# Kernel tuning notes

Hardware: AMD Instinct MI355X
Metric: run time of the kernel (lower is better)

Reference implementation:

```python
import jax, jax.numpy as jnp
import numpy as np
import math

M, DIN, DTGT = 65536, 256, 256   # feature count and feature dims
S, SD_IN, SD_TGT = 64, 256, 256  # num_slots, in_slot_dim, tgt_slot_dim
ITERS = 3
H_IN = 128                        # mlp_in hidden (hardcoded 128 in source)
H_TGT = SD_TGT if SD_TGT > 128 else 128  # mlp_tgt hidden

ARGS = ["inputs", "target", "in_slots", "tgt_slots",
        "ln_in_g", "ln_in_b", "ln_tgt_g", "ln_tgt_b",
        "Wk", "bk", "Wv", "bv", "Wvt", "bvt",
        "ln_slots_g", "ln_slots_b", "Wq", "bq",
        "gru_in_Wih", "gru_in_Whh", "gru_in_bih", "gru_in_bhh",
        "gru_tgt_Wih", "gru_tgt_Whh", "gru_tgt_bih", "gru_tgt_bhh",
        "ln_mi_g", "ln_mi_b", "mi_W1", "mi_b1", "mi_W2", "mi_b2",
        "ln_mt_g", "ln_mt_b", "mt_W1", "mt_b1", "mt_W2", "mt_b2"]


def _ln(x, g, b):
    m = jnp.mean(x, axis=-1, keepdims=True)
    v = jnp.var(x, axis=-1, keepdims=True)
    return (x - m) * jax.lax.rsqrt(v + 1e-5) * g + b


def _gru(x, h, Wih, Whh, bih, bhh):
    # torch.nn.GRUCell semantics; Wih: (D, 3H), Whh: (H, 3H)
    H = h.shape[-1]
    gi = x @ Wih + bih
    gh = h @ Whh + bhh
    r = jax.nn.sigmoid(gi[:, :H] + gh[:, :H])
    z = jax.nn.sigmoid(gi[:, H:2 * H] + gh[:, H:2 * H])
    n = jnp.tanh(gi[:, 2 * H:] + r * gh[:, 2 * H:])
    return (1.0 - z) * n + z * h


def _forward(inputs, target, in_slots, tgt_slots,
             ln_in_g, ln_in_b, ln_tgt_g, ln_tgt_b,
             Wk, bk, Wv, bv, Wvt, bvt,
             ln_slots_g, ln_slots_b, Wq, bq,
             gru_in_Wih, gru_in_Whh, gru_in_bih, gru_in_bhh,
             gru_tgt_Wih, gru_tgt_Whh, gru_tgt_bih, gru_tgt_bhh,
             ln_mi_g, ln_mi_b, mi_W1, mi_b1, mi_W2, mi_b2,
             ln_mt_g, ln_mt_b, mt_W1, mt_b1, mt_W2, mt_b2):
    inputs_norm = _ln(inputs, ln_in_g, ln_in_b)          # [M, DIN]
    in_k = inputs_norm @ Wk + bk                          # [M, SD_IN]
    in_v = inputs_norm @ Wv + bv                          # [M, SD_IN]
    tgt_v = _ln(target, ln_tgt_g, ln_tgt_b) @ Wvt + bvt   # [M, SD_TGT]
    scale = 1.0 / math.sqrt(in_k.shape[1])
    attn = None
    for _ in range(ITERS):
        q = _ln(in_slots, ln_slots_g, ln_slots_b) @ Wq + bq   # [S, SD_IN]
        logits = (q @ in_k.T) * scale                          # [S, M]
        attn = jax.nn.softmax(logits, axis=0)                  # softmax over SLOTS (dim=0)
        in_up = attn @ in_v                                    # [S, SD_IN]
        tgt_up = attn @ tgt_v                                  # [S, SD_TGT]
        in_slots = _gru(in_up, in_slots, gru_in_Wih, gru_in_Whh, gru_in_bih, gru_in_bhh)
        tgt_slots = _gru(tgt_up, tgt_slots, gru_tgt_Wih, gru_tgt_Whh, gru_tgt_bih, gru_tgt_bhh)
        in_slots = in_slots + (jax.nn.relu(_ln(in_slots, ln_mi_g, ln_mi_b) @ mi_W1 + mi_b1) @ mi_W2 + mi_b2)
        tgt_slots = tgt_slots + (jax.nn.relu(_ln(tgt_slots, ln_mt_g, ln_mt_b) @ mt_W1 + mt_b1) @ mt_W2 + mt_b2)
    return (in_slots, tgt_slots, attn)


def setup_inputs() -> dict:
    key = jax.random.key(0)
    ks = iter(jax.random.split(key, 64))
    rn = lambda shape, s=1.0: jax.random.normal(next(ks), shape, dtype=jnp.float32) * s
    w = 0.02
    d = {
        "inputs": rn((M, DIN)),
        "target": rn((M, DTGT)),
        "in_slots": rn((S, SD_IN)),
        "tgt_slots": rn((S, SD_TGT)),
        "ln_in_g": jnp.ones((DIN,)), "ln_in_b": jnp.zeros((DIN,)),
        "ln_tgt_g": jnp.ones((DTGT,)), "ln_tgt_b": jnp.zeros((DTGT,)),
        "Wk": rn((DIN, SD_IN), w), "bk": jnp.zeros((SD_IN,)),
        "Wv": rn((DIN, SD_IN), w), "bv": jnp.zeros((SD_IN,)),
        "Wvt": rn((DTGT, SD_TGT), w), "bvt": jnp.zeros((SD_TGT,)),
        "ln_slots_g": jnp.ones((SD_IN,)), "ln_slots_b": jnp.zeros((SD_IN,)),
        "Wq": rn((SD_IN, SD_IN), w), "bq": jnp.zeros((SD_IN,)),
        "gru_in_Wih": rn((SD_IN, 3 * SD_IN), w), "gru_in_Whh": rn((SD_IN, 3 * SD_IN), w),
        "gru_in_bih": jnp.zeros((3 * SD_IN,)), "gru_in_bhh": jnp.zeros((3 * SD_IN,)),
        "gru_tgt_Wih": rn((SD_TGT, 3 * SD_TGT), w), "gru_tgt_Whh": rn((SD_TGT, 3 * SD_TGT), w),
        "gru_tgt_bih": jnp.zeros((3 * SD_TGT,)), "gru_tgt_bhh": jnp.zeros((3 * SD_TGT,)),
        "ln_mi_g": jnp.ones((SD_IN,)), "ln_mi_b": jnp.zeros((SD_IN,)),
        "mi_W1": rn((SD_IN, H_IN), w), "mi_b1": jnp.zeros((H_IN,)),
        "mi_W2": rn((H_IN, SD_IN), w), "mi_b2": jnp.zeros((SD_IN,)),
        "ln_mt_g": jnp.ones((SD_TGT,)), "ln_mt_b": jnp.zeros((SD_TGT,)),
        "mt_W1": rn((SD_TGT, H_TGT), w), "mt_b1": jnp.zeros((H_TGT,)),
        "mt_W2": rn((H_TGT, SD_TGT), w), "mt_b2": jnp.zeros((SD_TGT,)),
    }
    return {k: d[k] for k in ARGS}


def reference(inputs, target, in_slots, tgt_slots,
              ln_in_g, ln_in_b, ln_tgt_g, ln_tgt_b,
              Wk, bk, Wv, bv, Wvt, bvt,
              ln_slots_g, ln_slots_b, Wq, bq,
              gru_in_Wih, gru_in_Whh, gru_in_bih, gru_in_bhh,
              gru_tgt_Wih, gru_tgt_Whh, gru_tgt_bih, gru_tgt_bhh,
              ln_mi_g, ln_mi_b, mi_W1, mi_b1, mi_W2, mi_b2,
              ln_mt_g, ln_mt_b, mt_W1, mt_b1, mt_W2, mt_b2):
    return _forward(inputs, target, in_slots, tgt_slots,
                    ln_in_g, ln_in_b, ln_tgt_g, ln_tgt_b,
                    Wk, bk, Wv, bv, Wvt, bvt,
                    ln_slots_g, ln_slots_b, Wq, bq,
                    gru_in_Wih, gru_in_Whh, gru_in_bih, gru_in_bhh,
                    gru_tgt_Wih, gru_tgt_Whh, gru_tgt_bih, gru_tgt_bhh,
                    ln_mi_g, ln_mi_b, mi_W1, mi_b1, mi_W2, mi_b2,
                    ln_mt_g, ln_mt_b, mt_W1, mt_b1, mt_W2, mt_b2)
```

## Files before the change

kernel.cpp:

```cpp
#include <hip/hip_runtime.h>
#include <hip/hip_bf16.h>
#include <math.h>

typedef __bf16 bf16_t;
typedef __bf16 bf16x8 __attribute__((ext_vector_type(8)));
typedef __bf16 bf16x4 __attribute__((ext_vector_type(4)));
typedef float f32x4 __attribute__((ext_vector_type(4)));

#define DEVI __device__ __forceinline__

DEVI f32x4 mfma16(bf16x8 a, bf16x8 b, f32x4 c) {
  return __builtin_amdgcn_mfma_f32_16x16x32_bf16(a, b, c, 0, 0, 0);
}
DEVI bf16x8 ld8(const bf16_t* p) { return *reinterpret_cast<const bf16x8*>(p); }


struct WtArgs { const float* s0; const float* s1; const float* s2; const float* s3;
                const float* s4; const float* s5; const float* s6; const float* s7;
                const float* s8; const float* s9; const float* s10; const float* s11; };

__global__ __launch_bounds__(256) void k_wtrans(WtArgs A, bf16_t* __restrict__ wt) {
  constexpr int offs[12] = {0,65536,131072,196608,262144,458752,655360,851968,
                            1048576,1081344,1114112,1179648};
  constexpr int Ks[12]   = {256,256,256,256,256,256,256,256,256,128,256,256};
  constexpr int Ns[12]   = {256,256,256,256,768,768,768,768,128,256,256,256};
  const int m = blockIdx.y;
  const int K = Ks[m], N = Ns[m];
  const int tn = N >> 6;
  const int tile = blockIdx.x;
  if (tile >= (K >> 6) * tn) return;
  const int tk = tile / tn, tc = tile - tk * tn;
  const float* sp;
  switch (m) {
    case 0: sp = A.s0; break; case 1: sp = A.s1; break; case 2: sp = A.s2; break;
    case 3: sp = A.s3; break; case 4: sp = A.s4; break; case 5: sp = A.s5; break;
    case 6: sp = A.s6; break; case 7: sp = A.s7; break; case 8: sp = A.s8; break;
    case 9: sp = A.s9; break; case 10: sp = A.s10; break; default: sp = A.s11; break;
  }
  __shared__ float ts[64][65];
  const int t = threadIdx.x;
  const int k0 = tk * 64, n0 = tc * 64;
  {
    const int c = t & 63, rq = t >> 6;
    #pragma unroll
    for (int i = 0; i < 16; ++i) {
      const int r = rq * 16 + i;
      ts[r][c] = sp[(size_t)(k0 + r) * N + n0 + c];
    }
  }
  __syncthreads();
  bf16_t* dst = wt + offs[m];
  const int n_l = t & 63, kq = t >> 6;
  #pragma unroll
  for (int h = 0; h < 2; ++h) {
    const int k_l = kq * 16 + h * 8;
    bf16x8 pk;
    #pragma unroll
    for (int e = 0; e < 8; ++e) pk[e] = (bf16_t)ts[k_l + e][n_l];
    const int n_g = n0 + n_l, k_g = k0 + k_l;
    const int nt = n_g >> 4, kc = k_g >> 5;
    const int lane = (((k_g >> 3) & 3) << 4) + (n_g & 15);
    *reinterpret_cast<bf16x8*>(dst + (((size_t)(nt * (K >> 5) + kc)) << 9) + lane * 8) = pk;
  }
}

__global__ __launch_bounds__(256) void k_init(const float* __restrict__ in_slots,
                                              const float* __restrict__ tgt_slots,
                                              float* __restrict__ h_f32,
                                              bf16_t* __restrict__ h_bf) {
  int idx = blockIdx.x * 256 + threadIdx.x;
  int side = idx >> 14, j = idx & 16383;
  int s = j >> 8, d = j & 255;
  float x = (side ? tgt_slots : in_slots)[j];
  h_f32[idx] = x;
  h_bf[side*16384 + (((s>>4)*8 + (d>>5))<<9) + ((d>>3)&3)*128 + (s&15)*8 + (d&7)] = (bf16_t)x;
}

__global__ __launch_bounds__(256) void k_phaseA(
    const float* __restrict__ inputs, const float* __restrict__ target,
    const float* __restrict__ ln_in_g, const float* __restrict__ ln_in_b,
    const float* __restrict__ ln_tgt_g, const float* __restrict__ ln_tgt_b,
    const bf16_t* __restrict__ wkF, const bf16_t* __restrict__ wvF, const bf16_t* __restrict__ wvtF,
    const float* __restrict__ bk, const float* __restrict__ bv, const float* __restrict__ bvt,
    bf16_t* __restrict__ in_kF, bf16_t* __restrict__ in_vF, bf16_t* __restrict__ tgt_vF) {
  const int side = blockIdx.y;
  const int m0 = blockIdx.x * 64;
  const int t = threadIdx.x, l = t & 63, w = t >> 6;
  __shared__ __align__(16) bf16_t anorm[64][264];
  const float* src = side ? target : inputs;
  const float* gp = side ? ln_tgt_g : ln_in_g;
  const float* bp = side ? ln_tgt_b : ln_in_b;
  const float4 g4 = *reinterpret_cast<const float4*>(gp + l * 4);
  const float4 b4 = *reinterpret_cast<const float4*>(bp + l * 4);
  float4 v[16];
  #pragma unroll
  for (int i = 0; i < 16; ++i)
    v[i] = *reinterpret_cast<const float4*>(src + (size_t)(m0 + w*16 + i) * 256 + l * 4);
  #pragma unroll
  for (int i = 0; i < 16; ++i) {
    float s1 = v[i].x + v[i].y + v[i].z + v[i].w;
    float s2 = v[i].x*v[i].x + v[i].y*v[i].y + v[i].z*v[i].z + v[i].w*v[i].w;
    #pragma unroll
    for (int msk = 1; msk < 64; msk <<= 1) { s1 += __shfl_xor(s1, msk); s2 += __shfl_xor(s2, msk); }
    const float mean = s1 * (1.f/256.f);
    const float rstd = rsqrtf(s2 * (1.f/256.f) - mean*mean + 1e-5f);
    bf16x4 pk;
    pk[0] = (bf16_t)((v[i].x - mean) * rstd * g4.x + b4.x);
    pk[1] = (bf16_t)((v[i].y - mean) * rstd * g4.y + b4.y);
    pk[2] = (bf16_t)((v[i].z - mean) * rstd * g4.z + b4.z);
    pk[3] = (bf16_t)((v[i].w - mean) * rstd * g4.w + b4.w);
    *reinterpret_cast<bf16x4*>(&anorm[w*16 + i][l*4]) = pk;
  }
  __syncthreads();
  const int l16 = l & 15, l4 = l >> 4;
  const int e = l16 & 7, lh = l16 >> 3;

  if (side == 0) {
    f32x4 acc[4][4] = {};
    for (int ks = 0; ks < 8; ++ks) {
      const int k = ks*32 + l4*8;
      bf16x8 a[4], b[4];
      #pragma unroll
      for (int mi = 0; mi < 4; ++mi) a[mi] = ld8(&anorm[mi*16 + l16][k]);
      #pragma unroll
      for (int ni = 0; ni < 4; ++ni) b[ni] = ld8(wkF + (((size_t)((w*4 + ni)*8 + ks)) << 9) + l*8);
      #pragma unroll
      for (int mi = 0; mi < 4; ++mi)
        #pragma unroll
        for (int ni = 0; ni < 4; ++ni) acc[mi][ni] = mfma16(a[mi], b[ni], acc[mi][ni]);
    }
    #pragma unroll
    for (int mi = 0; mi < 4; ++mi)
      #pragma unroll
      for (int ni = 0; ni < 4; ++ni) {
        const int d = w*64 + ni*16 + l16;
        const float bias = bk[d];
        const int kc = w*2 + (ni >> 1);
        const int l4p = (ni & 1)*2 + lh;
        bf16_t* outp = in_kF + ((((size_t)(blockIdx.x*4 + mi))*8 + kc) << 9) + l4p*128 + e;
        #pragma unroll
        for (int rr = 0; rr < 4; ++rr)
          outp[(l4*4 + rr)*8] = (bf16_t)(acc[mi][ni][rr] + bias);
      }
  }
  {
    const bf16_t* WF = side ? wvtF : wvF;
    const float* bias = side ? bvt : bv;
    bf16_t* out = side ? tgt_vF : in_vF;
    f32x4 acc[4][4] = {};
    for (int ks = 0; ks < 8; ++ks) {
      const int k = ks*32 + l4*8;
      bf16x8 a[4], b[4];
      #pragma unroll
      for (int mi = 0; mi < 4; ++mi) a[mi] = ld8(WF + (((size_t)((w*4 + mi)*8 + ks)) << 9) + l*8);
      #pragma unroll
      for (int ni = 0; ni < 4; ++ni) b[ni] = ld8(&anorm[ni*16 + l16][k]);
      #pragma unroll
      for (int mi = 0; mi < 4; ++mi)
        #pragma unroll
        for (int ni = 0; ni < 4; ++ni) acc[mi][ni] = mfma16(a[mi], b[ni], acc[mi][ni]);
    }
    #pragma unroll
    for (int mi = 0; mi < 4; ++mi)
      #pragma unroll
      for (int ni = 0; ni < 4; ++ni) {
        const int dt = w*4 + mi;
        const int mc = blockIdx.x*2 + (ni >> 1);
        const int l4p = (ni & 1)*2 + lh;
        bf16_t* outp = out + ((((size_t)dt)*2048 + mc) << 9) + l4p*128 + e;
        #pragma unroll
        for (int rr = 0; rr < 4; ++rr) {
          const int d = w*64 + mi*16 + l4*4 + rr;
          outp[(l4*4 + rr)*8] = (bf16_t)(acc[mi][ni][rr] + bias[d]);
        }
      }
  }
}

__global__ __launch_bounds__(256) void k_q(
    const float* __restrict__ h_in,
    const float* __restrict__ ln_g, const float* __restrict__ ln_b,
    const bf16_t* __restrict__ wqF, const float* __restrict__ bq,
    bf16_t* __restrict__ q_bf) {
  __shared__ __align__(16) bf16_t anorm[64][264];
  const int t = threadIdx.x, l = t & 63, w = t >> 6;
  const float4 g4 = *reinterpret_cast<const float4*>(ln_g + l * 4);
  const float4 b4 = *reinterpret_cast<const float4*>(ln_b + l * 4);
  float4 v[16];
  #pragma unroll
  for (int i = 0; i < 16; ++i)
    v[i] = *reinterpret_cast<const float4*>(h_in + (size_t)(w*16 + i) * 256 + l * 4);
  #pragma unroll
  for (int i = 0; i < 16; ++i) {
    float s1 = v[i].x + v[i].y + v[i].z + v[i].w;
    float s2 = v[i].x*v[i].x + v[i].y*v[i].y + v[i].z*v[i].z + v[i].w*v[i].w;
    #pragma unroll
    for (int msk = 1; msk < 64; msk <<= 1) { s1 += __shfl_xor(s1, msk); s2 += __shfl_xor(s2, msk); }
    const float mean = s1 * (1.f/256.f);
    const float rstd = rsqrtf(s2 * (1.f/256.f) - mean*mean + 1e-5f);
    bf16x4 pk;
    pk[0] = (bf16_t)((v[i].x - mean) * rstd * g4.x + b4.x);
    pk[1] = (bf16_t)((v[i].y - mean) * rstd * g4.y + b4.y);
    pk[2] = (bf16_t)((v[i].z - mean) * rstd * g4.z + b4.z);
    pk[3] = (bf16_t)((v[i].w - mean) * rstd * g4.w + b4.w);
    *reinterpret_cast<bf16x4*>(&anorm[w*16 + i][l*4]) = pk;
  }
  __syncthreads();
  const int l16 = l & 15, l4 = l >> 4;
  f32x4 acc[4][4] = {};
  for (int ks = 0; ks < 8; ++ks) {
    const int k = ks*32 + l4*8;
    bf16x8 a[4], b[4];
    #pragma unroll
    for (int mi = 0; mi < 4; ++mi) a[mi] = ld8(&anorm[mi*16 + l16][k]);
    #pragma unroll
    for (int ni = 0; ni < 4; ++ni) b[ni] = ld8(wqF + (((size_t)((w*4 + ni)*8 + ks)) << 9) + l*8);
    #pragma unroll
    for (int mi = 0; mi < 4; ++mi)
      #pragma unroll
      for (int ni = 0; ni < 4; ++ni) acc[mi][ni] = mfma16(a[mi], b[ni], acc[mi][ni]);
  }
  #pragma unroll
  for (int mi = 0; mi < 4; ++mi)
    #pragma unroll
    for (int ni = 0; ni < 4; ++ni) {
      const int d = w*64 + ni*16 + l16;
      const float bias = bq[d];
      bf16_t* outp = q_bf + (((size_t)(mi*8 + w*2 + (ni>>1))) << 9) + ((ni&1)*2 + (l16>>3))*128 + (l16&7);
      #pragma unroll
      for (int rr = 0; rr < 4; ++rr)
        outp[(l4*4 + rr)*8] = (bf16_t)((acc[mi][ni][rr] + bias) * 0.0625f);
    }
}

__global__ __launch_bounds__(256) void k_logits(
    const bf16_t* __restrict__ q_bf, const bf16_t* __restrict__ in_kF,
    bf16_t* __restrict__ attnF, float* __restrict__ attn_f32, int write_f32) {
  const int t = threadIdx.x, l = t & 63, w = t >> 6, l16 = l & 15, l4 = l >> 4;
  const int m0 = blockIdx.x * 256 + w * 64;
  f32x4 acc[4][4] = {};
  for (int ks = 0; ks < 8; ++ks) {
    bf16x8 a[4], b[4];
    #pragma unroll
    for (int mi = 0; mi < 4; ++mi) a[mi] = ld8(q_bf + (((size_t)(mi*8 + ks)) << 9) + l*8);
    #pragma unroll
    for (int ni = 0; ni < 4; ++ni)
      b[ni] = ld8(in_kF + (((size_t)((blockIdx.x*16 + w*4 + ni)*8 + ks)) << 9) + l*8);
    #pragma unroll
    for (int mi = 0; mi < 4; ++mi)
      #pragma unroll
      for (int ni = 0; ni < 4; ++ni) acc[mi][ni] = mfma16(a[mi], b[ni], acc[mi][ni]);
  }
  #pragma unroll
  for (int ni = 0; ni < 4; ++ni) {
    float mx = -3.0e38f;
    #pragma unroll
    for (int mi = 0; mi < 4; ++mi)
      #pragma unroll
      for (int rr = 0; rr < 4; ++rr) mx = fmaxf(mx, acc[mi][ni][rr]);
    mx = fmaxf(mx, __shfl_xor(mx, 16));
    mx = fmaxf(mx, __shfl_xor(mx, 32));
    float sm = 0.f;
    #pragma unroll
    for (int mi = 0; mi < 4; ++mi)
      #pragma unroll
      for (int rr = 0; rr < 4; ++rr) {
        float ev = __expf(acc[mi][ni][rr] - mx);
        acc[mi][ni][rr] = ev; sm += ev;
      }
    sm += __shfl_xor(sm, 16);
    sm += __shfl_xor(sm, 32);
    const float inv = 1.0f / sm;
    #pragma unroll
    for (int mi = 0; mi < 4; ++mi)
      #pragma unroll
      for (int rr = 0; rr < 4; ++rr) acc[mi][ni][rr] *= inv;
  }
  #pragma unroll
  for (int mi = 0; mi < 4; ++mi)
    #pragma unroll
    for (int ni = 0; ni < 4; ++ni) {
      const int mc = blockIdx.x*8 + w*2 + (ni >> 1);
      bf16_t* outp = attnF + ((((size_t)mi)*2048 + mc) << 9) + ((ni&1)*2 + (l16>>3))*128 + (l16&7);
      #pragma unroll
      for (int rr = 0; rr < 4; ++rr) {
        outp[(l4*4 + rr)*8] = (bf16_t)acc[mi][ni][rr];
        if (write_f32) {
          const int s = mi*16 + l4*4 + rr;
          attn_f32[(size_t)s*65536 + (m0 + ni*16 + l16)] = acc[mi][ni][rr];
        }
      }
    }
}

__global__ __launch_bounds__(256) void k_pv(
    const bf16_t* __restrict__ attnF,
    const bf16_t* __restrict__ in_vF, const bf16_t* __restrict__ tgt_vF,
    bf16_t* __restrict__ p_in, bf16_t* __restrict__ p_tgt) {
  const int c = blockIdx.x, side = blockIdx.y;
  const bf16_t* V = side ? tgt_vF : in_vF;
  bf16_t* P = side ? p_tgt : p_in;
  const int t = threadIdx.x, l = t & 63, w = t >> 6, l16 = l & 15, l4 = l >> 4;
  f32x4 acc[4][4] = {};
  for (int ks = 0; ks < 16; ++ks) {
    const size_t mc = c*16 + ks;
    bf16x8 a[4], b[4];
    #pragma unroll
    for (int mi = 0; mi < 4; ++mi) a[mi] = ld8(attnF + ((((size_t)mi)*2048 + mc) << 9) + l*8);
    #pragma unroll
    for (int ni = 0; ni < 4; ++ni) b[ni] = ld8(V + ((((size_t)(w*4 + ni))*2048 + mc) << 9) + l*8);
    #pragma unroll
    for (int mi = 0; mi < 4; ++mi)
      #pragma unroll
      for (int ni = 0; ni < 4; ++ni) acc[mi][ni] = mfma16(a[mi], b[ni], acc[mi][ni]);
  }
  #pragma unroll
  for (int mi = 0; mi < 4; ++mi)
    #pragma unroll
    for (int ni = 0; ni < 4; ++ni) {
      const int d = w*64 + ni*16 + l16;
      #pragma unroll
      for (int rr = 0; rr < 4; ++rr) {
        const int s = mi*16 + l4*4 + rr;
        P[(size_t)c*16384 + s*256 + d] = (bf16_t)acc[mi][ni][rr];
      }
    }
}

__global__ __launch_bounds__(256) void k_pvred(
    const bf16_t* __restrict__ p_in, const bf16_t* __restrict__ p_tgt,
    bf16_t* __restrict__ upF) {
  const int b = blockIdx.x;
  const int side = b >> 6, s = b & 63;
  const int d = threadIdx.x;
  const bf16_t* P = (side ? p_tgt : p_in) + s*256 + d;
  float sum = 0.f;
  #pragma unroll 8
  for (int cc = 0; cc < 128; ++cc) sum += (float)P[(size_t)cc * 16384];
  upF[side*16384 + (((s>>4)*8 + (d>>5))<<9) + ((d>>3)&3)*128 + (s&15)*8 + (d&7)] = (bf16_t)sum;
}

__global__ __launch_bounds__(256) void k_gates(
    const bf16_t* __restrict__ upF, const bf16_t* __restrict__ h_bf,
    const bf16_t* __restrict__ wihF_in, const bf16_t* __restrict__ whhF_in,
    const bf16_t* __restrict__ wihF_tgt, const bf16_t* __restrict__ whhF_tgt,
    const float* __restrict__ bih_in, const float* __restrict__ bhh_in,
    const float* __restrict__ bih_tgt, const float* __restrict__ bhh_tgt,
    float* __restrict__ gi, float* __restrict__ gh) {
  const int nchunk = blockIdx.x, which = blockIdx.y, side = blockIdx.z;
  const bf16_t* Aop = (which ? h_bf : upF) + side*16384;
  const bf16_t* WF = side ? (which ? whhF_tgt : wihF_tgt) : (which ? whhF_in : wihF_in);
  const float* bias = side ? (which ? bhh_tgt : bih_tgt) : (which ? bhh_in : bih_in);
  float* out = (which ? gh : gi) + side*49152;
  const int t = threadIdx.x, l = t & 63, w = t >> 6, l16 = l & 15, l4 = l >> 4;
  const int n0 = nchunk*256 + w*64;
  f32x4 acc[4][4] = {};
  for (int ks = 0; ks < 8; ++ks) {
    bf16x8 a[4], b[4];
    #pragma unroll
    for (int mi = 0; mi < 4; ++mi) a[mi] = ld8(Aop + (((size_t)(mi*8 + ks)) << 9) + l*8);
    #pragma unroll
    for (int ni = 0; ni < 4; ++ni)
      b[ni] = ld8(WF + (((size_t)((nchunk*16 + w*4 + ni)*8 + ks)) << 9) + l*8);
    #pragma unroll
    for (int mi = 0; mi < 4; ++mi)
      #pragma unroll
      for (int ni = 0; ni < 4; ++ni) acc[mi][ni] = mfma16(a[mi], b[ni], acc[mi][ni]);
  }
  #pragma unroll
  for (int mi = 0; mi < 4; ++mi)
    #pragma unroll
    for (int ni = 0; ni < 4; ++ni) {
      const int n = n0 + ni*16 + l16;
      const float bb = bias[n];
      #pragma unroll
      for (int rr = 0; rr < 4; ++rr) {
        const int s = mi*16 + l4*4 + rr;
        out[(size_t)s*768 + n] = acc[mi][ni][rr] + bb;
      }
    }
}

__global__ __launch_bounds__(256) void k_gru_ln(
    const float* __restrict__ gi, const float* __restrict__ gh,
    const float* __restrict__ h_f32,
    const float* __restrict__ ln_mi_g, const float* __restrict__ ln_mi_b,
    const float* __restrict__ ln_mt_g, const float* __restrict__ ln_mt_b,
    float* __restrict__ hp_f32, bf16_t* __restrict__ hpnF) {
  const int s = blockIdx.x, side = blockIdx.y;
  const int d = threadIdx.x;
  const float* GI = gi + side*49152 + s*768;
  const float* GH = gh + side*49152 + s*768;
  const float hv = h_f32[side*16384 + s*256 + d];
  const float rg = 1.f / (1.f + __expf(-(GI[d] + GH[d])));
  const float zg = 1.f / (1.f + __expf(-(GI[256 + d] + GH[256 + d])));
  const float ng = tanhf(GI[512 + d] + rg * GH[512 + d]);
  const float hp = (1.f - zg) * ng + zg * hv;
  float a = hp, b2 = hp * hp;
  #pragma unroll
  for (int msk = 1; msk < 64; msk <<= 1) { a += __shfl_xor(a, msk); b2 += __shfl_xor(b2, msk); }
  __shared__ float reda[4], redb[4];
  const int w = d >> 6, lid = d & 63;
  if (lid == 0) { reda[w] = a; redb[w] = b2; }
  __syncthreads();
  const float S1 = reda[0] + reda[1] + reda[2] + reda[3];
  const float S2 = redb[0] + redb[1] + redb[2] + redb[3];
  const float mean = S1 * (1.f/256.f);
  const float rstd = rsqrtf(S2 * (1.f/256.f) - mean*mean + 1e-5f);
  const float* g = side ? ln_mt_g : ln_mi_g;
  const float* bb = side ? ln_mt_b : ln_mi_b;
  const float nv = (hp - mean) * rstd * g[d] + bb[d];
  hp_f32[side*16384 + s*256 + d] = hp;
  hpnF[side*16384 + (((s>>4)*8 + (d>>5))<<9) + ((d>>3)&3)*128 + (s&15)*8 + (d&7)] = (bf16_t)nv;
}

__global__ __launch_bounds__(256) void k_mlpq(
    const bf16_t* __restrict__ hpnF,
    const bf16_t* __restrict__ w1F_in, const bf16_t* __restrict__ w1F_tgt,
    const float* __restrict__ b1_in, const float* __restrict__ b1_tgt,
    const bf16_t* __restrict__ w2F_in, const bf16_t* __restrict__ w2F_tgt,
    const float* __restrict__ b2_in, const float* __restrict__ b2_tgt,
    const float* __restrict__ hp_f32,
    float* __restrict__ h_f32, bf16_t* __restrict__ h_bf, float* __restrict__ slots_out,
    const float* __restrict__ ln_sg, const float* __restrict__ ln_sb,
    const bf16_t* __restrict__ wqF, const float* __restrict__ bq,
    bf16_t* __restrict__ q_bf, int make_q) {
  const int side = blockIdx.x;
  __shared__ __align__(16) bf16_t hid[64][264];
  const int t = threadIdx.x, l = t & 63, w = t >> 6, l16 = l & 15, l4 = l >> 4;
  const int NH = side ? 256 : 128;
  {
    const bf16_t* Aop = hpnF + side*16384;
    const bf16_t* WF = side ? w1F_tgt : w1F_in;
    const float* b1 = side ? b1_tgt : b1_in;
    const int ntiles = NH >> 6;
    for (int nt = 0; nt < ntiles; ++nt) {
      const int n0 = w*(NH>>2) + nt*16;
      f32x4 acc[4] = {};
      for (int ks = 0; ks < 8; ++ks) {
        bf16x8 b = ld8(WF + (((size_t)((n0>>4)*8 + ks)) << 9) + l*8);
        #pragma unroll
        for (int mt = 0; mt < 4; ++mt)
          acc[mt] = mfma16(ld8(Aop + (((size_t)(mt*8 + ks)) << 9) + l*8), b, acc[mt]);
      }
      const float bb = b1[n0 + l16];
      #pragma unroll
      for (int mt = 0; mt < 4; ++mt)
        #pragma unroll
        for (int rr = 0; rr < 4; ++rr) {
          const int s = mt*16 + l4*4 + rr;
          hid[s][n0 + l16] = (bf16_t)fmaxf(acc[mt][rr] + bb, 0.f);
        }
    }
  }
  __syncthreads();
  {
    const bf16_t* WF = side ? w2F_tgt : w2F_in;
    const float* b2 = side ? b2_tgt : b2_in;
    const int ksteps = NH >> 5;
    #pragma unroll
    for (int nt = 0; nt < 4; ++nt) {
      const int n0 = w*64 + nt*16;
      f32x4 acc[4] = {};
      for (int ks = 0; ks < ksteps; ++ks) {
        const int k = ks*32 + l4*8;
        bf16x8 b = ld8(WF + (((size_t)((n0>>4)*ksteps + ks)) << 9) + l*8);
        #pragma unroll
        for (int mt = 0; mt < 4; ++mt)
          acc[mt] = mfma16(ld8(&hid[mt*16 + l16][k]), b, acc[mt]);
      }
      const int n = n0 + l16;
      const float bb = b2[n];
      #pragma unroll
      for (int mt = 0; mt < 4; ++mt)
        #pragma unroll
        for (int rr = 0; rr < 4; ++rr) {
          const int s = mt*16 + l4*4 + rr;
          const int idx = side*16384 + s*256 + n;
          const float val = acc[mt][rr] + bb + hp_f32[idx];
          h_f32[idx] = val;
          slots_out[idx] = val;
          h_bf[side*16384 + (((s>>4)*8 + (n>>5))<<9) + ((n>>3)&3)*128 + (s&15)*8 + (n&7)] = (bf16_t)val;
        }
    }
  }
  if (!make_q || side != 0) return;
  __syncthreads();
  {
    for (int i = 0; i < 16; ++i) {
      const int s = w*16 + i;
      float4 x = *reinterpret_cast<const float4*>(h_f32 + s*256 + 4*l);
      float a = x.x + x.y + x.z + x.w;
      float b2s = x.x*x.x + x.y*x.y + x.z*x.z + x.w*x.w;
      #pragma unroll
      for (int msk = 1; msk < 64; msk <<= 1) { a += __shfl_xor(a, msk); b2s += __shfl_xor(b2s, msk); }
      const float mean = a * (1.f/256.f);
      const float rstd = rsqrtf(b2s * (1.f/256.f) - mean*mean + 1e-5f);
      float4 g4 = *reinterpret_cast<const float4*>(ln_sg + 4*l);
      float4 bb4 = *reinterpret_cast<const float4*>(ln_sb + 4*l);
      bf16x4 pk;
      pk[0] = (bf16_t)((x.x - mean) * rstd * g4.x + bb4.x);
      pk[1] = (bf16_t)((x.y - mean) * rstd * g4.y + bb4.y);
      pk[2] = (bf16_t)((x.z - mean) * rstd * g4.z + bb4.z);
      pk[3] = (bf16_t)((x.w - mean) * rstd * g4.w + bb4.w);
      *reinterpret_cast<bf16x4*>(&hid[s][4*l]) = pk;
    }
  }
  __syncthreads();
  {
    #pragma unroll
    for (int nt = 0; nt < 4; ++nt) {
      const int n0 = w*64 + nt*16;
      f32x4 acc[4] = {};
      for (int ks = 0; ks < 8; ++ks) {
        const int k = ks*32 + l4*8;
        bf16x8 b = ld8(wqF + (((size_t)((n0>>4)*8 + ks)) << 9) + l*8);
        #pragma unroll
        for (int mt = 0; mt < 4; ++mt)
          acc[mt] = mfma16(ld8(&hid[mt*16 + l16][k]), b, acc[mt]);
      }
      const int d = n0 + l16;
      const float bb = bq[d];
      bf16_t* outp = q_bf + (((size_t)(0)) ) ;
      #pragma unroll
      for (int mt = 0; mt < 4; ++mt) {
        bf16_t* op = q_bf + (((size_t)(mt*8 + (d>>5))) << 9) + ((d>>3)&3)*128 + (d&7);
        #pragma unroll
        for (int rr = 0; rr < 4; ++rr)
          op[(l4*4 + rr)*8] = (bf16_t)((acc[mt][rr] + bb) * 0.0625f);
      }
      (void)outp;
    }
  }
}

extern "C" void kernel_launch(void* const* d_in, const int* in_sizes, int n_in,
                              void* d_out, int out_size, void* d_ws, size_t ws_size,
                              hipStream_t stream) {
  (void)in_sizes; (void)n_in; (void)out_size; (void)ws_size;
  const float* inputs     = (const float*)d_in[0];
  const float* target     = (const float*)d_in[1];
  const float* in_slots   = (const float*)d_in[2];
  const float* tgt_slots  = (const float*)d_in[3];
  const float* ln_in_g    = (const float*)d_in[4];
  const float* ln_in_b    = (const float*)d_in[5];
  const float* ln_tgt_g   = (const float*)d_in[6];
  const float* ln_tgt_b   = (const float*)d_in[7];
  const float* Wk  = (const float*)d_in[8];
  const float* bk  = (const float*)d_in[9];
  const float* Wv  = (const float*)d_in[10];
  const float* bv  = (const float*)d_in[11];
  const float* Wvt = (const float*)d_in[12];
  const float* bvt = (const float*)d_in[13];
  const float* ln_slots_g = (const float*)d_in[14];
  const float* ln_slots_b = (const float*)d_in[15];
  const float* Wq  = (const float*)d_in[16];
  const float* bq  = (const float*)d_in[17];
  const float* gru_in_Wih  = (const float*)d_in[18];
  const float* gru_in_Whh  = (const float*)d_in[19];
  const float* gru_in_bih  = (const float*)d_in[20];
  const float* gru_in_bhh  = (const float*)d_in[21];
  const float* gru_tgt_Wih = (const float*)d_in[22];
  const float* gru_tgt_Whh = (const float*)d_in[23];
  const float* gru_tgt_bih = (const float*)d_in[24];
  const float* gru_tgt_bhh = (const float*)d_in[25];
  const float* ln_mi_g = (const float*)d_in[26];
  const float* ln_mi_b = (const float*)d_in[27];
  const float* mi_W1 = (const float*)d_in[28];
  const float* mi_b1 = (const float*)d_in[29];
  const float* mi_W2 = (const float*)d_in[30];
  const float* mi_b2 = (const float*)d_in[31];
  const float* ln_mt_g = (const float*)d_in[32];
  const float* ln_mt_b = (const float*)d_in[33];
  const float* mt_W1 = (const float*)d_in[34];
  const float* mt_b1 = (const float*)d_in[35];
  const float* mt_W2 = (const float*)d_in[36];
  const float* mt_b2 = (const float*)d_in[37];

  char* ws = (char*)d_ws;
  bf16_t* wt      = (bf16_t*)(ws);
  bf16_t* in_kF   = (bf16_t*)(ws + 2490368ull);
  bf16_t* in_vF   = (bf16_t*)(ws + 36044800ull);
  bf16_t* tgt_vF  = (bf16_t*)(ws + 69599232ull);
  bf16_t* attnF   = (bf16_t*)(ws + 103153664ull);
  bf16_t* q_bf    = (bf16_t*)(ws + 111542272ull);
  bf16_t* h_bf    = (bf16_t*)(ws + 111575040ull);
  bf16_t* upF     = (bf16_t*)(ws + 111640576ull);
  bf16_t* hpnF    = (bf16_t*)(ws + 111673344ull);
  float*  h_f32   = (float*)(ws + 111706112ull);
  float*  hp_f32  = (float*)(ws + 111837184ull);
  float*  gi      = (float*)(ws + 111968256ull);
  float*  gh      = (float*)(ws + 112361472ull);
  bf16_t* p_in    = (bf16_t*)(ws + 112754688ull);
  bf16_t* p_tgt   = (bf16_t*)(ws + 116948992ull);

  bf16_t* wkF = wt;
  bf16_t* wvF = wt + 65536;
  bf16_t* wvtF = wt + 131072;
  bf16_t* wqF = wt + 196608;
  bf16_t* wihF_in  = wt + 262144;
  bf16_t* whhF_in  = wt + 458752;
  bf16_t* wihF_tgt = wt + 655360;
  bf16_t* whhF_tgt = wt + 851968;
  bf16_t* w1F_in  = wt + 1048576;
  bf16_t* w2F_in  = wt + 1081344;
  bf16_t* w1F_tgt = wt + 1114112;
  bf16_t* w2F_tgt = wt + 1179648;

  float* attn_out = (float*)d_out + 32768;

  WtArgs wa = {Wk, Wv, Wvt, Wq, gru_in_Wih, gru_in_Whh, gru_tgt_Wih, gru_tgt_Whh,
               mi_W1, mi_W2, mt_W1, mt_W2};
  k_wtrans<<<dim3(48, 12), 256, 0, stream>>>(wa, wt);
  k_init<<<128, 256, 0, stream>>>(in_slots, tgt_slots, h_f32, h_bf);
  k_phaseA<<<dim3(1024, 2), 256, 0, stream>>>(inputs, target, ln_in_g, ln_in_b,
      ln_tgt_g, ln_tgt_b, wkF, wvF, wvtF, bk, bv, bvt, in_kF, in_vF, tgt_vF);
  k_q<<<1, 256, 0, stream>>>(h_f32, ln_slots_g, ln_slots_b, wqF, bq, q_bf);

  for (int it = 0; it < 3; ++it) {
    k_logits<<<256, 256, 0, stream>>>(q_bf, in_kF, attnF, attn_out, it == 2 ? 1 : 0);
    k_pv<<<dim3(128, 2), 256, 0, stream>>>(attnF, in_vF, tgt_vF, p_in, p_tgt);
    k_pvred<<<128, 256, 0, stream>>>(p_in, p_tgt, upF);
    k_gates<<<dim3(3, 2, 2), 256, 0, stream>>>(upF, h_bf, wihF_in, whhF_in,
        wihF_tgt, whhF_tgt, gru_in_bih, gru_in_bhh, gru_tgt_bih, gru_tgt_bhh, gi, gh);
    k_gru_ln<<<dim3(64, 2), 256, 0, stream>>>(gi, gh, h_f32, ln_mi_g, ln_mi_b,
        ln_mt_g, ln_mt_b, hp_f32, hpnF);
    k_mlpq<<<2, 256, 0, stream>>>(hpnF, w1F_in, w1F_tgt, mi_b1, mt_b1,
        w2F_in, w2F_tgt, mi_b2, mt_b2, hp_f32, h_f32, h_bf, (float*)d_out,
        ln_slots_g, ln_slots_b, wqF, bq, q_bf, it < 2 ? 1 : 0);
  }
}
```

Baseline: 330.3 us.

## Split layernorm and K/V projection into separate kernels via bf16 fragment buffer

Replaces the fused phaseA (layernorm plus projection through shared memory) with two kernels. The first writes normalized inputs and targets as bf16 in MFMA fragment layout to workspace. The second computes the K and V projections with register-blocked 4x4 MFMA tiles that load fragments directly from global memory. This removes the shared-memory staging and LDS traffic, at the cost of an extra 64 MB write and read round trip through HBM. The split path is taken only when the workspace is large enough.

```diff
diff --git a/kernel.cpp b/kernel.cpp
--- a/kernel.cpp
+++ b/kernel.cpp
@@ -74,6 +74,121 @@
   float x = (side ? tgt_slots : in_slots)[j];
   h_f32[idx] = x;
   h_bf[side*16384 + (((s>>4)*8 + (d>>5))<<9) + ((d>>3)&3)*128 + (s&15)*8 + (d&7)] = (bf16_t)x;
+}
+
+__global__ __launch_bounds__(256) void k_ln(
+    const float* __restrict__ inputs, const float* __restrict__ target,
+    const float* __restrict__ g_in, const float* __restrict__ b_in,
+    const float* __restrict__ g_tgt, const float* __restrict__ b_tgt,
+    bf16_t* __restrict__ anormF) {
+  const int wg = blockIdx.x * 4 + (threadIdx.x >> 6);
+  const int l = threadIdx.x & 63;
+  const int r0 = wg * 16;
+  const int side = r0 >> 16;
+  const int m0 = r0 & 65535;
+  const float* src = side ? target : inputs;
+  const float4 g4 = *reinterpret_cast<const float4*>((side ? g_tgt : g_in) + l*4);
+  const float4 b4 = *reinterpret_cast<const float4*>((side ? b_tgt : b_in) + l*4);
+  bf16_t* dst = anormF + (size_t)side * 16777216;
+  const int d = l * 4;
+  const size_t doff = (size_t)((d>>5) << 9) + ((d>>3)&3)*128 + (d&7);
+  #pragma unroll
+  for (int ii = 0; ii < 4; ++ii) {
+    float4 x[4];
+    #pragma unroll
+    for (int j = 0; j < 4; ++j)
+      x[j] = *reinterpret_cast<const float4*>(src + (size_t)(m0 + ii*4 + j)*256 + d);
+    #pragma unroll
+    for (int j = 0; j < 4; ++j) {
+      const int m = m0 + ii*4 + j;
+      float s1 = x[j].x + x[j].y + x[j].z + x[j].w;
+      float s2 = x[j].x*x[j].x + x[j].y*x[j].y + x[j].z*x[j].z + x[j].w*x[j].w;
+      #pragma unroll
+      for (int msk = 1; msk < 64; msk <<= 1) { s1 += __shfl_xor(s1, msk); s2 += __shfl_xor(s2, msk); }
+      const float mean = s1 * (1.f/256.f);
+      const float rstd = rsqrtf(s2 * (1.f/256.f) - mean*mean + 1e-5f);
+      bf16x4 pk;
+      pk[0] = (bf16_t)((x[j].x - mean) * rstd * g4.x + b4.x);
+      pk[1] = (bf16_t)((x[j].y - mean) * rstd * g4.y + b4.y);
+      pk[2] = (bf16_t)((x[j].z - mean) * rstd * g4.z + b4.z);
+      pk[3] = (bf16_t)((x[j].w - mean) * rstd * g4.w + b4.w);
+      *reinterpret_cast<bf16x4*>(dst + (size_t)(((m>>4)*8) << 9) + (m&15)*8 + doff) = pk;
+    }
+  }
+}
+
+__global__ __launch_bounds__(256) void k_proj(
+    const bf16_t* __restrict__ anormF,
+    const bf16_t* __restrict__ wkF, const bf16_t* __restrict__ wvF, const bf16_t* __restrict__ wvtF,
+    const float* __restrict__ bk, const float* __restrict__ bv, const float* __restrict__ bvt,
+    bf16_t* __restrict__ in_kF, bf16_t* __restrict__ in_vF, bf16_t* __restrict__ tgt_vF) {
+  const int side = blockIdx.y;
+  const int t = threadIdx.x, l = t & 63, w = t >> 6, l16 = l & 15, l4 = l >> 4;
+  const int e = l16 & 7, lh = l16 >> 3;
+  const bf16_t* aF = anormF + (size_t)side * 16777216;
+
+  if (side == 0) {
+    f32x4 acc[4][4] = {};
+    for (int ks = 0; ks < 8; ++ks) {
+      bf16x8 a[4], b[4];
+      #pragma unroll
+      for (int mi = 0; mi < 4; ++mi)
+        a[mi] = ld8(aF + (((size_t)((blockIdx.x*4 + mi)*8 + ks)) << 9) + l*8);
+      #pragma unroll
+      for (int ni = 0; ni < 4; ++ni)
+        b[ni] = ld8(wkF + (((size_t)((w*4 + ni)*8 + ks)) << 9) + l*8);
+      #pragma unroll
+      for (int mi = 0; mi < 4; ++mi)
+        #pragma unroll
+        for (int ni = 0; ni < 4; ++ni) acc[mi][ni] = mfma16(a[mi], b[ni], acc[mi][ni]);
+    }
+    #pragma unroll
+    for (int mi = 0; mi < 4; ++mi)
+      #pragma unroll
+      for (int ni = 0; ni < 4; ++ni) {
+        const int d = w*64 + ni*16 + l16;
+        const float bias = bk[d];
+        const int kc = w*2 + (ni >> 1);
+        const int l4p = (ni & 1)*2 + lh;
+        bf16_t* outp = in_kF + ((((size_t)(blockIdx.x*4 + mi))*8 + kc) << 9) + l4p*128 + e;
+        #pragma unroll
+        for (int rr = 0; rr < 4; ++rr)
+          outp[(l4*4 + rr)*8] = (bf16_t)(acc[mi][ni][rr] + bias);
+      }
+  }
+  {
+    const bf16_t* WF = side ? wvtF : wvF;
+    const float* bias = side ? bvt : bv;
+    bf16_t* out = side ? tgt_vF : in_vF;
+    f32x4 acc[4][4] = {};
+    for (int ks = 0; ks < 8; ++ks) {
+      bf16x8 a[4], b[4];
+      #pragma unroll
+      for (int mi = 0; mi < 4; ++mi)
+        a[mi] = ld8(WF + (((size_t)((w*4 + mi)*8 + ks)) << 9) + l*8);
+      #pragma unroll
+      for (int ni = 0; ni < 4; ++ni)
+        b[ni] = ld8(aF + (((size_t)((blockIdx.x*4 + ni)*8 + ks)) << 9) + l*8);
+      #pragma unroll
+      for (int mi = 0; mi < 4; ++mi)
+        #pragma unroll
+        for (int ni = 0; ni < 4; ++ni) acc[mi][ni] = mfma16(a[mi], b[ni], acc[mi][ni]);
+    }
+    #pragma unroll
+    for (int mi = 0; mi < 4; ++mi)
+      #pragma unroll
+      for (int ni = 0; ni < 4; ++ni) {
+        const int dt = w*4 + mi;
+        const int mc = blockIdx.x*2 + (ni >> 1);
+        const int l4p = (ni & 1)*2 + lh;
+        bf16_t* outp = out + ((((size_t)dt)*2048 + mc) << 9) + l4p*128 + e;
+        #pragma unroll
+        for (int rr = 0; rr < 4; ++rr) {
+          const int d = w*64 + mi*16 + l4*4 + rr;
+          outp[(l4*4 + rr)*8] = (bf16_t)(acc[mi][ni][rr] + bias[d]);
+        }
+      }
+  }
 }
 
 __global__ __launch_bounds__(256) void k_phaseA(
@@ -521,7 +636,6 @@
       }
       const int d = n0 + l16;
       const float bb = bq[d];
-      bf16_t* outp = q_bf + (((size_t)(0)) ) ;
       #pragma unroll
       for (int mt = 0; mt < 4; ++mt) {
         bf16_t* op = q_bf + (((size_t)(mt*8 + (d>>5))) << 9) + ((d>>3)&3)*128 + (d&7);
@@ -529,7 +643,6 @@
         for (int rr = 0; rr < 4; ++rr)
           op[(l4*4 + rr)*8] = (bf16_t)((acc[mt][rr] + bb) * 0.0625f);
       }
-      (void)outp;
     }
   }
 }
@@ -537,7 +650,7 @@
 extern "C" void kernel_launch(void* const* d_in, const int* in_sizes, int n_in,
                               void* d_out, int out_size, void* d_ws, size_t ws_size,
                               hipStream_t stream) {
-  (void)in_sizes; (void)n_in; (void)out_size; (void)ws_size;
+  (void)in_sizes; (void)n_in; (void)out_size;
   const float* inputs     = (const float*)d_in[0];
   const float* target     = (const float*)d_in[1];
   const float* in_slots   = (const float*)d_in[2];
@@ -593,6 +706,8 @@
   float*  gh      = (float*)(ws + 112361472ull);
   bf16_t* p_in    = (bf16_t*)(ws + 112754688ull);
   bf16_t* p_tgt   = (bf16_t*)(ws + 116948992ull);
+  bf16_t* anormF  = (bf16_t*)(ws + 121143296ull);
+  const bool use_split = ws_size >= 188252160ull;
 
   bf16_t* wkF = wt;
   bf16_t* wvF = wt + 65536;
@@ -613,8 +728,15 @@
                mi_W1, mi_W2, mt_W1, mt_W2};
   k_wtrans<<<dim3(48, 12), 256, 0, stream>>>(wa, wt);
   k_init<<<128, 256, 0, stream>>>(in_slots, tgt_slots, h_f32, h_bf);
-  k_phaseA<<<dim3(1024, 2), 256, 0, stream>>>(inputs, target, ln_in_g, ln_in_b,
-      ln_tgt_g, ln_tgt_b, wkF, wvF, wvtF, bk, bv, bvt, in_kF, in_vF, tgt_vF);
+  if (use_split) {
+    k_ln<<<2048, 256, 0, stream>>>(inputs, target, ln_in_g, ln_in_b,
+        ln_tgt_g, ln_tgt_b, anormF);
+    k_proj<<<dim3(1024, 2), 256, 0, stream>>>(anormF, wkF, wvF, wvtF,
+        bk, bv, bvt, in_kF, in_vF, tgt_vF);
+  } else {
+    k_phaseA<<<dim3(1024, 2), 256, 0, stream>>>(inputs, target, ln_in_g, ln_in_b,
+        ln_tgt_g, ln_tgt_b, wkF, wvF, wvtF, bk, bv, bvt, in_kF, in_vF, tgt_vF);
+  }
   k_q<<<1, 256, 0, stream>>>(h_f32, ln_slots_g, ln_slots_b, wqF, bq, q_bf);
 
   for (int it = 0; it < 3; ++it) {
```

Result: slower. 427.6 us (+29.5%).
